# Optimization experiments

Measured on AMD Instinct MI355X. Metric: run time of the kernel, lower is better.

The kernel has to match this reference:

```python
import jax, jax.numpy as jnp
import numpy as np

N = 100000
E = 3200000
N_IN = 256
N_OUT = 256


def setup_inputs() -> dict:
    key = jax.random.key(0)
    k1, k2, k3, k4, k5, k6 = jax.random.split(key, 6)
    x = jax.random.normal(k1, (N, N_IN), dtype=jnp.float32)
    edge_row = jax.random.randint(k2, (E,), 0, N, dtype=jnp.int32)
    edge_col = jax.random.randint(k3, (E,), 0, N, dtype=jnp.int32)
    edge_val = jax.random.uniform(k4, (E,), dtype=jnp.float32)
    # nn.Linear(n_in, n_out): weight [n_out, n_in], bias [n_out]
    bound = 1.0 / np.sqrt(N_IN)
    W = jax.random.uniform(k5, (N_OUT, N_IN), minval=-bound, maxval=bound, dtype=jnp.float32)
    b = jax.random.uniform(k6, (N_OUT,), minval=-bound, maxval=bound, dtype=jnp.float32)
    return {"x": x, "edge_row": edge_row, "edge_col": edge_col, "edge_val": edge_val, "W": W, "b": b}


def reference(x, edge_row, edge_col, edge_val, W, b):
    # linear projection: [N, n_out]
    h = x @ W.T + b
    # sparse adj @ h via gather + segment-sum: out[r] = sum_e val_e * h[c_e]
    msg = edge_val[:, None] * h[edge_col]          # [E, n_out]
    agg = jax.ops.segment_sum(msg, edge_row, num_segments=N)  # [N, n_out]
    return jax.nn.elu(agg)
```

## Files before the change

### kernel.cpp

```cpp
#include <hip/hip_runtime.h>
#include <hip/hip_bf16.h>


#define NF 256
#define NBLK 256
#define BSHIFT 9
#define BROWS 512
#define NBUCK_MAX 256
#define YSTR 264

typedef unsigned short u16;
typedef unsigned int u32;
typedef __attribute__((ext_vector_type(8))) short bf16x8;
typedef __attribute__((ext_vector_type(8))) u16 u16x8;
typedef __attribute__((ext_vector_type(4))) float f32x4;

__device__ __forceinline__ u16 f2bf(float f) {
    unsigned u = __float_as_uint(f);
    u = (u + 0x7fffu + ((u >> 16) & 1u)) >> 16;
    return (u16)u;
}
__device__ __forceinline__ float bf2f(u16 h) {
    return __uint_as_float(((unsigned)h) << 16);
}

__global__ __launch_bounds__(256) void cvt_kernel(const float* __restrict__ in,
                                                  u16* __restrict__ outv, long n) {
    long i = ((long)blockIdx.x * blockDim.x + threadIdx.x) * 4;
    long stride = (long)gridDim.x * blockDim.x * 4;
    for (; i < n; i += stride) {
        float4 f = *(const float4*)(in + i);
        ushort4 o;
        o.x = f2bf(f.x); o.y = f2bf(f.y); o.z = f2bf(f.z); o.w = f2bf(f.w);
        *(ushort4*)(outv + i) = o;
    }
}

__global__ __launch_bounds__(256) void quant_kernel(const float* __restrict__ x,
                                                    char* __restrict__ xq,
                                                    float* __restrict__ sarr, int n) {
    int wv = (int)(((long)blockIdx.x * 256 + threadIdx.x) >> 6);
    int lane = threadIdx.x & 63;
    if (wv >= n) return;
    const float* xp = x + (size_t)wv * NF;
    float4 f = *(const float4*)(xp + lane * 4);
    float m = fmaxf(fmaxf(fabsf(f.x), fabsf(f.y)), fmaxf(fabsf(f.z), fabsf(f.w)));
    #pragma unroll
    for (int off = 32; off; off >>= 1) m = fmaxf(m, __shfl_xor(m, off));
    float mm = fmaxf(m, 1e-20f);
    float rs = 127.f / mm;
    char4 q;
    q.x = (char)__float2int_rn(f.x * rs);
    q.y = (char)__float2int_rn(f.y * rs);
    q.z = (char)__float2int_rn(f.z * rs);
    q.w = (char)__float2int_rn(f.w * rs);
    ((char4*)(xq + (size_t)wv * NF))[lane] = q;
    if (lane == 0) sarr[wv] = mm / 127.f;
}

__global__ __launch_bounds__(256) void hist_kernel(const int* __restrict__ erow,
                                                   int* __restrict__ histG,
                                                   int E, int chunk, int nbuck) {
    __shared__ int h[NBUCK_MAX];
    int b = blockIdx.x, tid = threadIdx.x;
    for (int i = tid; i < nbuck; i += 256) h[i] = 0;
    __syncthreads();
    int s = b * chunk, e = min(E, s + chunk);
    for (int i = s + tid; i < e; i += 256)
        atomicAdd(&h[erow[i] >> BSHIFT], 1);
    __syncthreads();
    for (int i = tid; i < nbuck; i += 256) histG[i * NBLK + b] = h[i];
}

__global__ __launch_bounds__(256) void scanA(int* __restrict__ data,
                                             int* __restrict__ bsum, int n) {
    __shared__ int s[256];
    int tid = threadIdx.x;
    int i = blockIdx.x * 256 + tid;
    int v = (i < n) ? data[i] : 0;
    s[tid] = v;
    __syncthreads();
    #pragma unroll
    for (int off = 1; off < 256; off <<= 1) {
        int t = (tid >= off) ? s[tid - off] : 0;
        __syncthreads();
        s[tid] += t;
        __syncthreads();
    }
    if (i < n) data[i] = s[tid] - v;
    if (tid == 255) bsum[blockIdx.x] = s[255];
}

__global__ __launch_bounds__(512) void scanB(const int* __restrict__ bsum,
                                             int* __restrict__ boff, int nb,
                                             int* __restrict__ total_out) {
    __shared__ int s[512];
    int tid = threadIdx.x;
    int v = (tid < nb) ? bsum[tid] : 0;
    s[tid] = v;
    __syncthreads();
    #pragma unroll
    for (int off = 1; off < 512; off <<= 1) {
        int t = (tid >= off) ? s[tid - off] : 0;
        __syncthreads();
        s[tid] += t;
        __syncthreads();
    }
    if (tid < nb) boff[tid] = s[tid] - v;
    if (tid == 511) *total_out = s[511];
}

__global__ __launch_bounds__(256) void scanC(int* __restrict__ data,
                                             const int* __restrict__ boff, int n) {
    int i = blockIdx.x * 256 + threadIdx.x;
    if (i < n) data[i] += boff[blockIdx.x];
}

__global__ __launch_bounds__(256) void binscatter_kernel(
        const int* __restrict__ erow, const int* __restrict__ ecol,
        const float* __restrict__ eval, const int* __restrict__ histGs,
        int2* __restrict__ tmp, int E, int chunk, int nbuck) {
    __shared__ int cur[NBUCK_MAX];
    int b = blockIdx.x, tid = threadIdx.x;
    for (int i = tid; i < nbuck; i += 256) cur[i] = histGs[i * NBLK + b];
    __syncthreads();
    int s = b * chunk, e = min(E, s + chunk);
    for (int i = s + tid; i < e; i += 256) {
        int r = erow[i];
        int k = r >> BSHIFT;
        int pos = atomicAdd(&cur[k], 1);
        tmp[pos] = make_int2((r & (BROWS - 1)) | (ecol[i] << BSHIFT),
                             __float_as_int(eval[i]));
    }
}

__global__ __launch_bounds__(256) void cluster_fill_kernel(
        const int2* __restrict__ tmp, const int* __restrict__ histGs,
        int* __restrict__ row_ptr, u32* __restrict__ rec,
        int N, int E, int nbuck) {
    __shared__ int cnt[BROWS];
    __shared__ int cur[BROWS];
    int k = blockIdx.x, tid = threadIdx.x;
    int base = k << BSHIFT;
    int nrows = min(BROWS, N - base);
    int tstart = histGs[k * NBLK];
    int tend = (k + 1 < nbuck) ? histGs[(k + 1) * NBLK] : E;

    for (int i = tid; i < BROWS; i += 256) cnt[i] = 0;
    __syncthreads();
    for (int j = tstart + tid; j < tend; j += 256)
        atomicAdd(&cnt[((u32)tmp[j].x) & (BROWS - 1)], 1);
    __syncthreads();
    cur[tid] = cnt[tid];
    cur[tid + 256] = cnt[tid + 256];
    __syncthreads();
    #pragma unroll
    for (int off = 1; off < BROWS; off <<= 1) {
        int i0 = tid, i1 = tid + 256;
        int t0 = (i0 >= off) ? cur[i0 - off] : 0;
        int t1 = (i1 >= off) ? cur[i1 - off] : 0;
        __syncthreads();
        cur[i0] += t0; cur[i1] += t1;
        __syncthreads();
    }
    #pragma unroll
    for (int p = 0; p < 2; ++p) {
        int i = tid + p * 256;
        int excl = tstart + cur[i] - cnt[i];
        if (i < nrows) row_ptr[base + i] = excl;
        cur[i] = excl;
    }
    if (k == nbuck - 1 && tid == 0) row_ptr[N] = E;
    __syncthreads();
    for (int j = tstart + tid; j < tend; j += 256) {
        int2 t = tmp[j];
        u32 w = (u32)t.x;
        int rl = w & (BROWS - 1);
        u32 c = w >> BSHIFT;
        float v = __int_as_float(t.y);
        int v15 = (int)(v * 32768.f + 0.5f);
        if (v15 > 32767) v15 = 32767;
        int pos = atomicAdd(&cur[rl], 1);
        rec[pos] = c | ((u32)v15 << 17);
    }
}

#define ACCQ(hh, vv)                                                         \
    a0 += (vv) * (float)(char)((hh).x);        a1 += (vv) * (float)(char)((hh).x >> 8); \
    a2 += (vv) * (float)(char)((hh).x >> 16);  a3 += (vv) * (float)(char)((hh).x >> 24); \
    a4 += (vv) * (float)(char)((hh).y);        a5 += (vv) * (float)(char)((hh).y >> 8); \
    a6 += (vv) * (float)(char)((hh).y >> 16);  a7 += (vv) * (float)(char)((hh).y >> 24);

__global__ __launch_bounds__(512) void fused_kernel(
        const char* __restrict__ xq, const float* __restrict__ sarr,
        const int* __restrict__ row_ptr, const u32* __restrict__ rec,
        const u16* __restrict__ Wb, const float* __restrict__ bias,
        float* __restrict__ out, int n) {
    __shared__ u16 ys[16 * YSTR];
    __shared__ float ss[16];
    int tid = threadIdx.x;
    int wid = tid >> 6;
    int lane = tid & 63;
    int half = lane >> 5;
    int fl = lane & 31;
    int rbase = blockIdx.x * 16;
    const float VS = 1.f / 32768.f;
    const char* xbase = xq + fl * 8;

    #pragma unroll
    for (int rr = 0; rr < 2; ++rr) {
        int lr = wid * 2 + rr;
        int row = rbase + lr;
        int start = 0, end = 0;
        if (row < n) { start = row_ptr[row]; end = row_ptr[row + 1]; }
        float a0 = 0.f, a1 = 0.f, a2 = 0.f, a3 = 0.f;
        float a4 = 0.f, a5 = 0.f, a6 = 0.f, a7 = 0.f;
        float sv = 0.f;
        int j = start;
        for (; j + 8 <= end; j += 8) {
            u32 w0 = rec[j + half];
            u32 w1 = rec[j + 2 + half];
            u32 w2 = rec[j + 4 + half];
            u32 w3 = rec[j + 6 + half];
            u32 c0 = w0 & 0x1FFFF, c1 = w1 & 0x1FFFF;
            u32 c2 = w2 & 0x1FFFF, c3 = w3 & 0x1FFFF;
            uint2 h0 = *(const uint2*)(xbase + (size_t)c0 * NF);
            uint2 h1 = *(const uint2*)(xbase + (size_t)c1 * NF);
            uint2 h2 = *(const uint2*)(xbase + (size_t)c2 * NF);
            uint2 h3 = *(const uint2*)(xbase + (size_t)c3 * NF);
            float s0 = sarr[c0], s1 = sarr[c1], s2 = sarr[c2], s3 = sarr[c3];
            float v0 = (float)(w0 >> 17) * VS;
            float v1 = (float)(w1 >> 17) * VS;
            float v2 = (float)(w2 >> 17) * VS;
            float v3 = (float)(w3 >> 17) * VS;
            sv += (v0 + v1) + (v2 + v3);
            float g0 = v0 * s0, g1 = v1 * s1, g2 = v2 * s2, g3 = v3 * s3;
            ACCQ(h0, g0); ACCQ(h1, g1); ACCQ(h2, g2); ACCQ(h3, g3);
        }
        for (int jj = j + half; jj < end; jj += 2) {
            u32 w = rec[jj];
            u32 c = w & 0x1FFFF;
            uint2 h = *(const uint2*)(xbase + (size_t)c * NF);
            float v = (float)(w >> 17) * VS;
            float g = v * sarr[c];
            sv += v;
            ACCQ(h, g);
        }
        a0 += __shfl_xor(a0, 32); a1 += __shfl_xor(a1, 32);
        a2 += __shfl_xor(a2, 32); a3 += __shfl_xor(a3, 32);
        a4 += __shfl_xor(a4, 32); a5 += __shfl_xor(a5, 32);
        a6 += __shfl_xor(a6, 32); a7 += __shfl_xor(a7, 32);
        sv += __shfl_xor(sv, 32);
        if (half == 0) {
            u16x8 p;
            p[0] = f2bf(a0); p[1] = f2bf(a1); p[2] = f2bf(a2); p[3] = f2bf(a3);
            p[4] = f2bf(a4); p[5] = f2bf(a5); p[6] = f2bf(a6); p[7] = f2bf(a7);
            *(u16x8*)(&ys[lr * YSTR + fl * 8]) = p;
            if (fl == 0) ss[lr] = sv;
        }
    }
    __syncthreads();

    int lrow = lane & 15;
    int kgrp = lane >> 4;
    bf16x8 af[8];
    #pragma unroll
    for (int ks = 0; ks < 8; ++ks)
        af[ks] = *(const bf16x8*)(&ys[lrow * YSTR + ks * 32 + kgrp * 8]);
    float sj[4];
    #pragma unroll
    for (int r = 0; r < 4; ++r) sj[r] = ss[kgrp * 4 + r];

    #pragma unroll
    for (int t = 0; t < 2; ++t) {
        int o0 = wid * 32 + t * 16;
        const u16* wrow = Wb + (size_t)(o0 + lrow) * NF + kgrp * 8;
        f32x4 acc = {0.f, 0.f, 0.f, 0.f};
        #pragma unroll
        for (int ks = 0; ks < 8; ++ks) {
            bf16x8 bf = *(const bf16x8*)(wrow + ks * 32);
            acc = __builtin_amdgcn_mfma_f32_16x16x32_bf16(af[ks], bf, acc, 0, 0, 0);
        }
        float bo = bias[o0 + lrow];
        #pragma unroll
        for (int r = 0; r < 4; ++r) {
            int grow = rbase + kgrp * 4 + r;
            if (grow < n) {
                float v = acc[r] + sj[r] * bo;
                out[(size_t)grow * NF + o0 + lrow] = (v > 0.f) ? v : (__expf(v) - 1.f);
            }
        }
    }
}

__global__ __launch_bounds__(256) void agg_f32_kernel(
        const float* __restrict__ xf, const int* __restrict__ row_ptr,
        const u32* __restrict__ rec, float* __restrict__ yf,
        float* __restrict__ svec, int n) {
    int wv = (int)(((long)blockIdx.x * 256 + threadIdx.x) >> 6);
    int lane = threadIdx.x & 63;
    if (wv >= n) return;
    int start = row_ptr[wv];
    int end = row_ptr[wv + 1];
    const float VS = 1.f / 32768.f;
    const float4* xv = (const float4*)xf;
    float4 acc = make_float4(0.f, 0.f, 0.f, 0.f);
    float sv = 0.f;
    for (int j = start; j < end; ++j) {
        u32 w = rec[j];
        float v = (float)(w >> 17) * VS;
        float4 h = xv[(size_t)(w & 0x1FFFF) * 64 + lane];
        acc.x += v * h.x; acc.y += v * h.y;
        acc.z += v * h.z; acc.w += v * h.w;
        sv += v;
    }
    *(float4*)(yf + (size_t)wv * NF + lane * 4) = acc;
    if (lane == 0) svec[wv] = sv;
}

__global__ __launch_bounds__(256) void gemm_elu_f32_kernel(
        float* __restrict__ out, const u16* __restrict__ Wb,
        const float* __restrict__ bias, const float* __restrict__ svec, int n) {
    int wid = threadIdx.x >> 6;
    int lane = threadIdx.x & 63;
    int lrow = lane & 15;
    int kgrp = lane >> 4;
    int r0 = blockIdx.x * 128 + wid * 32;
    if (r0 >= n) return;
    int rowA = min(r0 + lrow, n - 1);
    int rowB = min(r0 + 16 + lrow, n - 1);
    bf16x8 afA[8], afB[8];
    const float* yA = (const float*)out + (size_t)rowA * NF;
    const float* yB = (const float*)out + (size_t)rowB * NF;
    #pragma unroll
    for (int ks = 0; ks < 8; ++ks) {
        int k0 = ks * 32 + kgrp * 8;
        float4 f0 = *(const float4*)(yA + k0);
        float4 f1 = *(const float4*)(yA + k0 + 4);
        bf16x8 a;
        a[0] = (short)f2bf(f0.x); a[1] = (short)f2bf(f0.y);
        a[2] = (short)f2bf(f0.z); a[3] = (short)f2bf(f0.w);
        a[4] = (short)f2bf(f1.x); a[5] = (short)f2bf(f1.y);
        a[6] = (short)f2bf(f1.z); a[7] = (short)f2bf(f1.w);
        afA[ks] = a;
        f0 = *(const float4*)(yB + k0);
        f1 = *(const float4*)(yB + k0 + 4);
        a[0] = (short)f2bf(f0.x); a[1] = (short)f2bf(f0.y);
        a[2] = (short)f2bf(f0.z); a[3] = (short)f2bf(f0.w);
        a[4] = (short)f2bf(f1.x); a[5] = (short)f2bf(f1.y);
        a[6] = (short)f2bf(f1.z); a[7] = (short)f2bf(f1.w);
        afB[ks] = a;
    }
    float sjA[4], sjB[4];
    #pragma unroll
    for (int r = 0; r < 4; ++r) {
        sjA[r] = svec[min(r0 + kgrp * 4 + r, n - 1)];
        sjB[r] = svec[min(r0 + 16 + kgrp * 4 + r, n - 1)];
    }
    for (int ot = 0; ot < 16; ++ot) {
        int o0 = ot * 16;
        const u16* wrow = Wb + (size_t)(o0 + lrow) * NF + kgrp * 8;
        f32x4 accA = {0.f, 0.f, 0.f, 0.f};
        f32x4 accB = {0.f, 0.f, 0.f, 0.f};
        #pragma unroll
        for (int ks = 0; ks < 8; ++ks) {
            bf16x8 bf = *(const bf16x8*)(wrow + ks * 32);
            accA = __builtin_amdgcn_mfma_f32_16x16x32_bf16(afA[ks], bf, accA, 0, 0, 0);
            accB = __builtin_amdgcn_mfma_f32_16x16x32_bf16(afB[ks], bf, accB, 0, 0, 0);
        }
        float bo = bias[o0 + lrow];
        #pragma unroll
        for (int r = 0; r < 4; ++r) {
            int ra = r0 + kgrp * 4 + r;
            if (ra < n) {
                float v = accA[r] + sjA[r] * bo;
                out[(size_t)ra * NF + o0 + lrow] = (v > 0.f) ? v : (__expf(v) - 1.f);
            }
            int rb = r0 + 16 + kgrp * 4 + r;
            if (rb < n) {
                float v = accB[r] + sjB[r] * bo;
                out[(size_t)rb * NF + o0 + lrow] = (v > 0.f) ? v : (__expf(v) - 1.f);
            }
        }
    }
}

extern "C" void kernel_launch(void* const* d_in, const int* in_sizes, int n_in,
                              void* d_out, int out_size, void* d_ws, size_t ws_size,
                              hipStream_t stream) {
    const float* x        = (const float*)d_in[0];
    const int*   edge_row = (const int*)d_in[1];
    const int*   edge_col = (const int*)d_in[2];
    const float* edge_val = (const float*)d_in[3];
    const float* W        = (const float*)d_in[4];
    const float* b        = (const float*)d_in[5];
    float* out = (float*)d_out;

    const int N = in_sizes[0] / NF;
    const int E = in_sizes[1];
    const int nbuck = (N + BROWS - 1) >> BSHIFT;
    const int chunk = (E + NBLK - 1) / NBLK;

    size_t off = 0;
    char* base = (char*)d_ws;
    auto take = [&](size_t bytes) -> char* {
        char* q = base + off;
        off += (bytes + 255) & ~(size_t)255;
        return q;
    };
    u32*   rec     = (u32*)take((size_t)E * 4);
    int*   row_ptr = (int*)take((size_t)(N + 1) * 4);
    int*   histG   = (int*)take((size_t)nbuck * NBLK * 4);
    int*   bsum    = (int*)take(1024 * 4);
    int*   boff    = (int*)take(1024 * 4);
    int*   scr     = (int*)take(256);
    float* svec    = (float*)take((size_t)N * 4);
    u16*   Wb      = (u16*)take((size_t)NF * NF * 2);
    float* sarr    = (float*)take((size_t)N * 4);
    int2*  tmp     = (int2*)take((size_t)E * 8);
    size_t preQ = off;
    char*  xq      = (char*)take((size_t)N * NF);
    bool useQ = off <= ws_size;
    (void)preQ;

    const int nHist = nbuck * NBLK;
    const int nHistBlk = (nHist + 255) / 256;

    cvt_kernel<<<64, 256, 0, stream>>>(W, Wb, (long)NF * NF);

    if (useQ)
        quant_kernel<<<(N + 3) / 4, 256, 0, stream>>>(x, xq, sarr, N);

    hist_kernel<<<NBLK, 256, 0, stream>>>(edge_row, histG, E, chunk, nbuck);
    scanA<<<nHistBlk, 256, 0, stream>>>(histG, bsum, nHist);
    scanB<<<1, 512, 0, stream>>>(bsum, boff, nHistBlk, scr);
    scanC<<<nHistBlk, 256, 0, stream>>>(histG, boff, nHist);
    binscatter_kernel<<<NBLK, 256, 0, stream>>>(edge_row, edge_col, edge_val,
                                                histG, tmp, E, chunk, nbuck);
    cluster_fill_kernel<<<nbuck, 256, 0, stream>>>(tmp, histG, row_ptr, rec,
                                                   N, E, nbuck);

    if (useQ) {
        fused_kernel<<<(N + 15) / 16, 512, 0, stream>>>(xq, sarr, row_ptr, rec,
                                                        Wb, b, out, N);
    } else {
        agg_f32_kernel<<<(N + 3) / 4, 256, 0, stream>>>(x, row_ptr, rec, out,
                                                        svec, N);
        gemm_elu_f32_kernel<<<(N + 127) / 128, 256, 0, stream>>>(out, Wb, b,
                                                                 svec, N);
    }
}
```

Measured before the change: 372.2 us.

## Sort edges by column segment within row buckets and fuse prep kernels

The edge binning key becomes (row bucket, column segment), so within each row bucket the edges are grouped by column range. This is meant to improve gather locality of quantized feature rows during aggregation. The quantize, weight-convert and histogram kernels are merged into one launch to cut launch overhead. The prefix scan gains an extra level to handle the larger histogram. Features switch to unsigned 8-bit with a +128 offset that is subtracted after accumulation, which makes the byte-to-float conversion cheaper. In exchange, the histogram is much larger (4096 keys in shared memory per block) and the scan chain now has more launches.

```diff
diff --git a/kernel.cpp b/kernel.cpp
--- a/kernel.cpp
+++ b/kernel.cpp
@@ -6,11 +6,13 @@
 #define NBLK 256
 #define BSHIFT 9
 #define BROWS 512
-#define NBUCK_MAX 256
+#define SEGSHIFT 13
+#define NKEY_MAX 4096
 #define YSTR 264
 
 typedef unsigned short u16;
 typedef unsigned int u32;
+typedef unsigned char u8;
 typedef __attribute__((ext_vector_type(8))) short bf16x8;
 typedef __attribute__((ext_vector_type(8))) u16 u16x8;
 typedef __attribute__((ext_vector_type(4))) float f32x4;
@@ -20,8 +22,55 @@
     u = (u + 0x7fffu + ((u >> 16) & 1u)) >> 16;
     return (u16)u;
 }
-__device__ __forceinline__ float bf2f(u16 h) {
-    return __uint_as_float(((unsigned)h) << 16);
+
+__global__ __launch_bounds__(256) void prep_kernel(
+        const float* __restrict__ x, u8* __restrict__ xq,
+        float* __restrict__ sarr, int n,
+        const float* __restrict__ W, u16* __restrict__ Wb,
+        const int* __restrict__ erow, const int* __restrict__ ecol,
+        int* __restrict__ histG, int E, int chunk, int nkeys, int nseg) {
+    __shared__ int h[NKEY_MAX];
+    int b = blockIdx.x, tid = threadIdx.x;
+    int QB = (n + 3) / 4;
+    if (b < QB) {
+        int wv = b * 4 + (tid >> 6);
+        int lane = tid & 63;
+        if (wv >= n) return;
+        const float* xp = x + (size_t)wv * NF;
+        float4 f = *(const float4*)(xp + lane * 4);
+        float m = fmaxf(fmaxf(fabsf(f.x), fabsf(f.y)),
+                        fmaxf(fabsf(f.z), fabsf(f.w)));
+        #pragma unroll
+        for (int off = 32; off; off >>= 1) m = fmaxf(m, __shfl_xor(m, off));
+        float mm = fmaxf(m, 1e-20f);
+        float rs = 127.f / mm;
+        uchar4 q;
+        q.x = (u8)(__float2int_rn(f.x * rs) + 128);
+        q.y = (u8)(__float2int_rn(f.y * rs) + 128);
+        q.z = (u8)(__float2int_rn(f.z * rs) + 128);
+        q.w = (u8)(__float2int_rn(f.w * rs) + 128);
+        ((uchar4*)(xq + (size_t)wv * NF))[lane] = q;
+        if (lane == 0) sarr[wv] = mm / 127.f;
+    } else if (b < QB + 64) {
+        long i = ((long)(b - QB) * 256 + tid) * 4;
+        if (i < (long)NF * NF) {
+            float4 f = *(const float4*)(W + i);
+            ushort4 o;
+            o.x = f2bf(f.x); o.y = f2bf(f.y); o.z = f2bf(f.z); o.w = f2bf(f.w);
+            *(ushort4*)(Wb + i) = o;
+        }
+    } else {
+        int hb = b - QB - 64;
+        for (int i = tid; i < nkeys; i += 256) h[i] = 0;
+        __syncthreads();
+        int s = hb * chunk, e = min(E, s + chunk);
+        for (int i = s + tid; i < e; i += 256) {
+            int key = (erow[i] >> BSHIFT) * nseg + (ecol[i] >> SEGSHIFT);
+            atomicAdd(&h[key], 1);
+        }
+        __syncthreads();
+        for (int i = tid; i < nkeys; i += 256) histG[i * NBLK + hb] = h[i];
+    }
 }
 
 __global__ __launch_bounds__(256) void cvt_kernel(const float* __restrict__ in,
@@ -36,40 +85,20 @@
     }
 }
 
-__global__ __launch_bounds__(256) void quant_kernel(const float* __restrict__ x,
-                                                    char* __restrict__ xq,
-                                                    float* __restrict__ sarr, int n) {
-    int wv = (int)(((long)blockIdx.x * 256 + threadIdx.x) >> 6);
-    int lane = threadIdx.x & 63;
-    if (wv >= n) return;
-    const float* xp = x + (size_t)wv * NF;
-    float4 f = *(const float4*)(xp + lane * 4);
-    float m = fmaxf(fmaxf(fabsf(f.x), fabsf(f.y)), fmaxf(fabsf(f.z), fabsf(f.w)));
-    #pragma unroll
-    for (int off = 32; off; off >>= 1) m = fmaxf(m, __shfl_xor(m, off));
-    float mm = fmaxf(m, 1e-20f);
-    float rs = 127.f / mm;
-    char4 q;
-    q.x = (char)__float2int_rn(f.x * rs);
-    q.y = (char)__float2int_rn(f.y * rs);
-    q.z = (char)__float2int_rn(f.z * rs);
-    q.w = (char)__float2int_rn(f.w * rs);
-    ((char4*)(xq + (size_t)wv * NF))[lane] = q;
-    if (lane == 0) sarr[wv] = mm / 127.f;
-}
-
-__global__ __launch_bounds__(256) void hist_kernel(const int* __restrict__ erow,
-                                                   int* __restrict__ histG,
-                                                   int E, int chunk, int nbuck) {
-    __shared__ int h[NBUCK_MAX];
+__global__ __launch_bounds__(256) void hist_kernel(
+        const int* __restrict__ erow, const int* __restrict__ ecol,
+        int* __restrict__ histG, int E, int chunk, int nkeys, int nseg) {
+    __shared__ int h[NKEY_MAX];
     int b = blockIdx.x, tid = threadIdx.x;
-    for (int i = tid; i < nbuck; i += 256) h[i] = 0;
+    for (int i = tid; i < nkeys; i += 256) h[i] = 0;
     __syncthreads();
     int s = b * chunk, e = min(E, s + chunk);
-    for (int i = s + tid; i < e; i += 256)
-        atomicAdd(&h[erow[i] >> BSHIFT], 1);
-    __syncthreads();
-    for (int i = tid; i < nbuck; i += 256) histG[i * NBLK + b] = h[i];
+    for (int i = s + tid; i < e; i += 256) {
+        int key = (erow[i] >> BSHIFT) * nseg + (ecol[i] >> SEGSHIFT);
+        atomicAdd(&h[key], 1);
+    }
+    __syncthreads();
+    for (int i = tid; i < nkeys; i += 256) histG[i * NBLK + b] = h[i];
 }
 
 __global__ __launch_bounds__(256) void scanA(int* __restrict__ data,
@@ -119,17 +148,18 @@
 __global__ __launch_bounds__(256) void binscatter_kernel(
         const int* __restrict__ erow, const int* __restrict__ ecol,
         const float* __restrict__ eval, const int* __restrict__ histGs,
-        int2* __restrict__ tmp, int E, int chunk, int nbuck) {
-    __shared__ int cur[NBUCK_MAX];
+        int2* __restrict__ tmp, int E, int chunk, int nkeys, int nseg) {
+    __shared__ int cur[NKEY_MAX];
     int b = blockIdx.x, tid = threadIdx.x;
-    for (int i = tid; i < nbuck; i += 256) cur[i] = histGs[i * NBLK + b];
+    for (int i = tid; i < nkeys; i += 256) cur[i] = histGs[i * NBLK + b];
     __syncthreads();
     int s = b * chunk, e = min(E, s + chunk);
     for (int i = s + tid; i < e; i += 256) {
         int r = erow[i];
-        int k = r >> BSHIFT;
-        int pos = atomicAdd(&cur[k], 1);
-        tmp[pos] = make_int2((r & (BROWS - 1)) | (ecol[i] << BSHIFT),
+        int c = ecol[i];
+        int key = (r >> BSHIFT) * nseg + (c >> SEGSHIFT);
+        int pos = atomicAdd(&cur[key], 1);
+        tmp[pos] = make_int2((r & (BROWS - 1)) | (c << BSHIFT),
                              __float_as_int(eval[i]));
     }
 }
@@ -137,14 +167,14 @@
 __global__ __launch_bounds__(256) void cluster_fill_kernel(
         const int2* __restrict__ tmp, const int* __restrict__ histGs,
         int* __restrict__ row_ptr, u32* __restrict__ rec,
-        int N, int E, int nbuck) {
+        int N, int E, int nbuck, int nseg) {
     __shared__ int cnt[BROWS];
     __shared__ int cur[BROWS];
     int k = blockIdx.x, tid = threadIdx.x;
     int base = k << BSHIFT;
     int nrows = min(BROWS, N - base);
-    int tstart = histGs[k * NBLK];
-    int tend = (k + 1 < nbuck) ? histGs[(k + 1) * NBLK] : E;
+    int tstart = histGs[(k * nseg) * NBLK];
+    int tend = (k + 1 < nbuck) ? histGs[((k + 1) * nseg) * NBLK] : E;
 
     for (int i = tid; i < BROWS; i += 256) cnt[i] = 0;
     __syncthreads();
@@ -185,14 +215,19 @@
     }
 }
 
-#define ACCQ(hh, vv)                                                         \
-    a0 += (vv) * (float)(char)((hh).x);        a1 += (vv) * (float)(char)((hh).x >> 8); \
-    a2 += (vv) * (float)(char)((hh).x >> 16);  a3 += (vv) * (float)(char)((hh).x >> 24); \
-    a4 += (vv) * (float)(char)((hh).y);        a5 += (vv) * (float)(char)((hh).y >> 8); \
-    a6 += (vv) * (float)(char)((hh).y >> 16);  a7 += (vv) * (float)(char)((hh).y >> 24);
+#define ACCU(hh, gg)                                                          \
+    a0 += (gg) * (float)((hh).x & 0xffu);                                     \
+    a1 += (gg) * (float)(((hh).x >> 8) & 0xffu);                              \
+    a2 += (gg) * (float)(((hh).x >> 16) & 0xffu);                             \
+    a3 += (gg) * (float)((hh).x >> 24);                                       \
+    a4 += (gg) * (float)((hh).y & 0xffu);                                     \
+    a5 += (gg) * (float)(((hh).y >> 8) & 0xffu);                              \
+    a6 += (gg) * (float)(((hh).y >> 16) & 0xffu);                             \
+    a7 += (gg) * (float)((hh).y >> 24);                                       \
+    t  += (gg);
 
 __global__ __launch_bounds__(512) void fused_kernel(
-        const char* __restrict__ xq, const float* __restrict__ sarr,
+        const u8* __restrict__ xq, const float* __restrict__ sarr,
         const int* __restrict__ row_ptr, const u32* __restrict__ rec,
         const u16* __restrict__ Wb, const float* __restrict__ bias,
         float* __restrict__ out, int n) {
@@ -205,7 +240,7 @@
     int fl = lane & 31;
     int rbase = blockIdx.x * 16;
     const float VS = 1.f / 32768.f;
-    const char* xbase = xq + fl * 8;
+    const u8* xbase = xq + fl * 8;
 
     #pragma unroll
     for (int rr = 0; rr < 2; ++rr) {
@@ -215,7 +250,7 @@
         if (row < n) { start = row_ptr[row]; end = row_ptr[row + 1]; }
         float a0 = 0.f, a1 = 0.f, a2 = 0.f, a3 = 0.f;
         float a4 = 0.f, a5 = 0.f, a6 = 0.f, a7 = 0.f;
-        float sv = 0.f;
+        float sv = 0.f, t = 0.f;
         int j = start;
         for (; j + 8 <= end; j += 8) {
             u32 w0 = rec[j + half];
@@ -235,7 +270,7 @@
             float v3 = (float)(w3 >> 17) * VS;
             sv += (v0 + v1) + (v2 + v3);
             float g0 = v0 * s0, g1 = v1 * s1, g2 = v2 * s2, g3 = v3 * s3;
-            ACCQ(h0, g0); ACCQ(h1, g1); ACCQ(h2, g2); ACCQ(h3, g3);
+            ACCU(h0, g0); ACCU(h1, g1); ACCU(h2, g2); ACCU(h3, g3);
         }
         for (int jj = j + half; jj < end; jj += 2) {
             u32 w = rec[jj];
@@ -244,8 +279,11 @@
             float v = (float)(w >> 17) * VS;
             float g = v * sarr[c];
             sv += v;
-            ACCQ(h, g);
-        }
+            ACCU(h, g);
+        }
+        float t128 = 128.f * t;
+        a0 -= t128; a1 -= t128; a2 -= t128; a3 -= t128;
+        a4 -= t128; a5 -= t128; a6 -= t128; a7 -= t128;
         a0 += __shfl_xor(a0, 32); a1 += __shfl_xor(a1, 32);
         a2 += __shfl_xor(a2, 32); a3 += __shfl_xor(a3, 32);
         a4 += __shfl_xor(a4, 32); a5 += __shfl_xor(a5, 32);
@@ -399,6 +437,8 @@
     const int N = in_sizes[0] / NF;
     const int E = in_sizes[1];
     const int nbuck = (N + BROWS - 1) >> BSHIFT;
+    const int nseg  = (N + (1 << SEGSHIFT) - 1) >> SEGSHIFT;
+    const int nkeys = nbuck * nseg;
     const int chunk = (E + NBLK - 1) / NBLK;
 
     size_t off = 0;
@@ -410,35 +450,43 @@
     };
     u32*   rec     = (u32*)take((size_t)E * 4);
     int*   row_ptr = (int*)take((size_t)(N + 1) * 4);
-    int*   histG   = (int*)take((size_t)nbuck * NBLK * 4);
-    int*   bsum    = (int*)take(1024 * 4);
-    int*   boff    = (int*)take(1024 * 4);
+    int*   histG   = (int*)take((size_t)nkeys * NBLK * 4);
+    int*   bsum1   = (int*)take((size_t)((nkeys * NBLK + 255) / 256) * 4);
+    int*   bsum2   = (int*)take(1024 * 4);
+    int*   boff2   = (int*)take(1024 * 4);
     int*   scr     = (int*)take(256);
     float* svec    = (float*)take((size_t)N * 4);
     u16*   Wb      = (u16*)take((size_t)NF * NF * 2);
     float* sarr    = (float*)take((size_t)N * 4);
     int2*  tmp     = (int2*)take((size_t)E * 8);
-    size_t preQ = off;
-    char*  xq      = (char*)take((size_t)N * NF);
+    u8*    xq      = (u8*)take((size_t)N * NF);
     bool useQ = off <= ws_size;
-    (void)preQ;
-
-    const int nHist = nbuck * NBLK;
-    const int nHistBlk = (nHist + 255) / 256;
-
-    cvt_kernel<<<64, 256, 0, stream>>>(W, Wb, (long)NF * NF);
-
-    if (useQ)
-        quant_kernel<<<(N + 3) / 4, 256, 0, stream>>>(x, xq, sarr, N);
-
-    hist_kernel<<<NBLK, 256, 0, stream>>>(edge_row, histG, E, chunk, nbuck);
-    scanA<<<nHistBlk, 256, 0, stream>>>(histG, bsum, nHist);
-    scanB<<<1, 512, 0, stream>>>(bsum, boff, nHistBlk, scr);
-    scanC<<<nHistBlk, 256, 0, stream>>>(histG, boff, nHist);
+
+    const int nHist = nkeys * NBLK;
+    const int nb1 = (nHist + 255) / 256;
+    const int nb2 = (nb1 + 255) / 256;
+
+    if (useQ) {
+        int QB = (N + 3) / 4;
+        prep_kernel<<<QB + 64 + NBLK, 256, 0, stream>>>(
+            x, xq, sarr, N, W, Wb, edge_row, edge_col, histG, E, chunk,
+            nkeys, nseg);
+    } else {
+        cvt_kernel<<<64, 256, 0, stream>>>(W, Wb, (long)NF * NF);
+        hist_kernel<<<NBLK, 256, 0, stream>>>(edge_row, edge_col, histG, E,
+                                              chunk, nkeys, nseg);
+    }
+
+    scanA<<<nb1, 256, 0, stream>>>(histG, bsum1, nHist);
+    scanA<<<nb2, 256, 0, stream>>>(bsum1, bsum2, nb1);
+    scanB<<<1, 512, 0, stream>>>(bsum2, boff2, nb2, scr);
+    scanC<<<nb2, 256, 0, stream>>>(bsum1, boff2, nb1);
+    scanC<<<nb1, 256, 0, stream>>>(histG, bsum1, nHist);
+
     binscatter_kernel<<<NBLK, 256, 0, stream>>>(edge_row, edge_col, edge_val,
-                                                histG, tmp, E, chunk, nbuck);
+                                                histG, tmp, E, chunk, nkeys, nseg);
     cluster_fill_kernel<<<nbuck, 256, 0, stream>>>(tmp, histG, row_ptr, rec,
-                                                   N, E, nbuck);
+                                                   N, E, nbuck, nseg);
 
     if (useQ) {
         fused_kernel<<<(N + 15) / 16, 512, 0, stream>>>(xq, sarr, row_ptr, rec,
```

New measurement: 406.7 us. 1.09x slower.

## Fuse prep kernels and shrink edge bucket temp to packed u32 plus u16

Applied to the files above, without the earlier changes.

Quantization of x, the W to bf16 conversion and the edge-row histogram now run as one launch, with blocks partitioned by role, instead of three separate kernels. The binning scatter now writes the final packed record (column plus 15-bit value) and a separate u16 local row, replacing the 8-byte int2 temp. The fill kernel therefore reads 6 bytes per edge instead of 8 and copies the record directly. The fill kernel also uses 512 threads so each thread owns one row slot. This cuts launch overhead and intermediate traffic, at the cost of two scattered writes per edge in binscatter.

```diff
diff --git a/kernel.cpp b/kernel.cpp
--- a/kernel.cpp
+++ b/kernel.cpp
@@ -11,6 +11,7 @@
 
 typedef unsigned short u16;
 typedef unsigned int u32;
+typedef unsigned char u8;
 typedef __attribute__((ext_vector_type(8))) short bf16x8;
 typedef __attribute__((ext_vector_type(8))) u16 u16x8;
 typedef __attribute__((ext_vector_type(4))) float f32x4;
@@ -20,8 +21,53 @@
     u = (u + 0x7fffu + ((u >> 16) & 1u)) >> 16;
     return (u16)u;
 }
-__device__ __forceinline__ float bf2f(u16 h) {
-    return __uint_as_float(((unsigned)h) << 16);
+
+__global__ __launch_bounds__(256) void prep_kernel(
+        const float* __restrict__ x, char* __restrict__ xq,
+        float* __restrict__ sarr, int n,
+        const float* __restrict__ W, u16* __restrict__ Wb,
+        const int* __restrict__ erow, int* __restrict__ histG,
+        int E, int chunk, int nbuck) {
+    __shared__ int h[NBUCK_MAX];
+    int b = blockIdx.x, tid = threadIdx.x;
+    int QB = (n + 3) / 4;
+    if (b < QB) {
+        int wv = b * 4 + (tid >> 6);
+        int lane = tid & 63;
+        if (wv >= n) return;
+        const float* xp = x + (size_t)wv * NF;
+        float4 f = *(const float4*)(xp + lane * 4);
+        float m = fmaxf(fmaxf(fabsf(f.x), fabsf(f.y)),
+                        fmaxf(fabsf(f.z), fabsf(f.w)));
+        #pragma unroll
+        for (int off = 32; off; off >>= 1) m = fmaxf(m, __shfl_xor(m, off));
+        float mm = fmaxf(m, 1e-20f);
+        float rs = 127.f / mm;
+        char4 q;
+        q.x = (char)__float2int_rn(f.x * rs);
+        q.y = (char)__float2int_rn(f.y * rs);
+        q.z = (char)__float2int_rn(f.z * rs);
+        q.w = (char)__float2int_rn(f.w * rs);
+        ((char4*)(xq + (size_t)wv * NF))[lane] = q;
+        if (lane == 0) sarr[wv] = mm / 127.f;
+    } else if (b < QB + 64) {
+        long i = ((long)(b - QB) * 256 + tid) * 4;
+        if (i < (long)NF * NF) {
+            float4 f = *(const float4*)(W + i);
+            ushort4 o;
+            o.x = f2bf(f.x); o.y = f2bf(f.y); o.z = f2bf(f.z); o.w = f2bf(f.w);
+            *(ushort4*)(Wb + i) = o;
+        }
+    } else {
+        int hb = b - QB - 64;
+        for (int i = tid; i < nbuck; i += 256) h[i] = 0;
+        __syncthreads();
+        int s = hb * chunk, e = min(E, s + chunk);
+        for (int i = s + tid; i < e; i += 256)
+            atomicAdd(&h[erow[i] >> BSHIFT], 1);
+        __syncthreads();
+        for (int i = tid; i < nbuck; i += 256) histG[i * NBLK + hb] = h[i];
+    }
 }
 
 __global__ __launch_bounds__(256) void cvt_kernel(const float* __restrict__ in,
@@ -36,28 +82,6 @@
     }
 }
 
-__global__ __launch_bounds__(256) void quant_kernel(const float* __restrict__ x,
-                                                    char* __restrict__ xq,
-                                                    float* __restrict__ sarr, int n) {
-    int wv = (int)(((long)blockIdx.x * 256 + threadIdx.x) >> 6);
-    int lane = threadIdx.x & 63;
-    if (wv >= n) return;
-    const float* xp = x + (size_t)wv * NF;
-    float4 f = *(const float4*)(xp + lane * 4);
-    float m = fmaxf(fmaxf(fabsf(f.x), fabsf(f.y)), fmaxf(fabsf(f.z), fabsf(f.w)));
-    #pragma unroll
-    for (int off = 32; off; off >>= 1) m = fmaxf(m, __shfl_xor(m, off));
-    float mm = fmaxf(m, 1e-20f);
-    float rs = 127.f / mm;
-    char4 q;
-    q.x = (char)__float2int_rn(f.x * rs);
-    q.y = (char)__float2int_rn(f.y * rs);
-    q.z = (char)__float2int_rn(f.z * rs);
-    q.w = (char)__float2int_rn(f.w * rs);
-    ((char4*)(xq + (size_t)wv * NF))[lane] = q;
-    if (lane == 0) sarr[wv] = mm / 127.f;
-}
-
 __global__ __launch_bounds__(256) void hist_kernel(const int* __restrict__ erow,
                                                    int* __restrict__ histG,
                                                    int E, int chunk, int nbuck) {
@@ -119,7 +143,8 @@
 __global__ __launch_bounds__(256) void binscatter_kernel(
         const int* __restrict__ erow, const int* __restrict__ ecol,
         const float* __restrict__ eval, const int* __restrict__ histGs,
-        int2* __restrict__ tmp, int E, int chunk, int nbuck) {
+        u32* __restrict__ tmp4, u16* __restrict__ rowlo,
+        int E, int chunk, int nbuck) {
     __shared__ int cur[NBUCK_MAX];
     int b = blockIdx.x, tid = threadIdx.x;
     for (int i = tid; i < nbuck; i += 256) cur[i] = histGs[i * NBLK + b];
@@ -128,16 +153,19 @@
     for (int i = s + tid; i < e; i += 256) {
         int r = erow[i];
         int k = r >> BSHIFT;
+        float v = eval[i];
+        int v15 = (int)(v * 32768.f + 0.5f);
+        if (v15 > 32767) v15 = 32767;
         int pos = atomicAdd(&cur[k], 1);
-        tmp[pos] = make_int2((r & (BROWS - 1)) | (ecol[i] << BSHIFT),
-                             __float_as_int(eval[i]));
-    }
-}
-
-__global__ __launch_bounds__(256) void cluster_fill_kernel(
-        const int2* __restrict__ tmp, const int* __restrict__ histGs,
-        int* __restrict__ row_ptr, u32* __restrict__ rec,
-        int N, int E, int nbuck) {
+        tmp4[pos] = (u32)ecol[i] | ((u32)v15 << 17);
+        rowlo[pos] = (u16)(r & (BROWS - 1));
+    }
+}
+
+__global__ __launch_bounds__(512) void cluster_fill_kernel(
+        const u32* __restrict__ tmp4, const u16* __restrict__ rowlo,
+        const int* __restrict__ histGs, int* __restrict__ row_ptr,
+        u32* __restrict__ rec, int N, int E, int nbuck) {
     __shared__ int cnt[BROWS];
     __shared__ int cur[BROWS];
     int k = blockIdx.x, tid = threadIdx.x;
@@ -146,42 +174,29 @@
     int tstart = histGs[k * NBLK];
     int tend = (k + 1 < nbuck) ? histGs[(k + 1) * NBLK] : E;
 
-    for (int i = tid; i < BROWS; i += 256) cnt[i] = 0;
-    __syncthreads();
-    for (int j = tstart + tid; j < tend; j += 256)
-        atomicAdd(&cnt[((u32)tmp[j].x) & (BROWS - 1)], 1);
+    cnt[tid] = 0;
+    __syncthreads();
+    for (int j = tstart + tid; j < tend; j += 512)
+        atomicAdd(&cnt[rowlo[j]], 1);
     __syncthreads();
     cur[tid] = cnt[tid];
-    cur[tid + 256] = cnt[tid + 256];
     __syncthreads();
     #pragma unroll
     for (int off = 1; off < BROWS; off <<= 1) {
-        int i0 = tid, i1 = tid + 256;
-        int t0 = (i0 >= off) ? cur[i0 - off] : 0;
-        int t1 = (i1 >= off) ? cur[i1 - off] : 0;
-        __syncthreads();
-        cur[i0] += t0; cur[i1] += t1;
-        __syncthreads();
-    }
-    #pragma unroll
-    for (int p = 0; p < 2; ++p) {
-        int i = tid + p * 256;
-        int excl = tstart + cur[i] - cnt[i];
-        if (i < nrows) row_ptr[base + i] = excl;
-        cur[i] = excl;
-    }
+        int t = (tid >= off) ? cur[tid - off] : 0;
+        __syncthreads();
+        cur[tid] += t;
+        __syncthreads();
+    }
+    int excl = tstart + cur[tid] - cnt[tid];
+    if (tid < nrows) row_ptr[base + tid] = excl;
+    cur[tid] = excl;
     if (k == nbuck - 1 && tid == 0) row_ptr[N] = E;
     __syncthreads();
-    for (int j = tstart + tid; j < tend; j += 256) {
-        int2 t = tmp[j];
-        u32 w = (u32)t.x;
-        int rl = w & (BROWS - 1);
-        u32 c = w >> BSHIFT;
-        float v = __int_as_float(t.y);
-        int v15 = (int)(v * 32768.f + 0.5f);
-        if (v15 > 32767) v15 = 32767;
+    for (int j = tstart + tid; j < tend; j += 512) {
+        int rl = rowlo[j];
         int pos = atomicAdd(&cur[rl], 1);
-        rec[pos] = c | ((u32)v15 << 17);
+        rec[pos] = tmp4[j];
     }
 }
 
@@ -417,28 +432,31 @@
     float* svec    = (float*)take((size_t)N * 4);
     u16*   Wb      = (u16*)take((size_t)NF * NF * 2);
     float* sarr    = (float*)take((size_t)N * 4);
-    int2*  tmp     = (int2*)take((size_t)E * 8);
-    size_t preQ = off;
+    u32*   tmp4    = (u32*)take((size_t)E * 4);
+    u16*   rowlo   = (u16*)take((size_t)E * 2);
     char*  xq      = (char*)take((size_t)N * NF);
     bool useQ = off <= ws_size;
-    (void)preQ;
 
     const int nHist = nbuck * NBLK;
-    const int nHistBlk = (nHist + 255) / 256;
-
-    cvt_kernel<<<64, 256, 0, stream>>>(W, Wb, (long)NF * NF);
-
-    if (useQ)
-        quant_kernel<<<(N + 3) / 4, 256, 0, stream>>>(x, xq, sarr, N);
-
-    hist_kernel<<<NBLK, 256, 0, stream>>>(edge_row, histG, E, chunk, nbuck);
-    scanA<<<nHistBlk, 256, 0, stream>>>(histG, bsum, nHist);
-    scanB<<<1, 512, 0, stream>>>(bsum, boff, nHistBlk, scr);
-    scanC<<<nHistBlk, 256, 0, stream>>>(histG, boff, nHist);
+    const int nb1 = (nHist + 255) / 256;
+
+    if (useQ) {
+        int QB = (N + 3) / 4;
+        prep_kernel<<<QB + 64 + NBLK, 256, 0, stream>>>(
+            x, xq, sarr, N, W, Wb, edge_row, histG, E, chunk, nbuck);
+    } else {
+        cvt_kernel<<<64, 256, 0, stream>>>(W, Wb, (long)NF * NF);
+        hist_kernel<<<NBLK, 256, 0, stream>>>(edge_row, histG, E, chunk, nbuck);
+    }
+
+    scanA<<<nb1, 256, 0, stream>>>(histG, bsum, nHist);
+    scanB<<<1, 512, 0, stream>>>(bsum, boff, nb1, scr);
+    scanC<<<nb1, 256, 0, stream>>>(histG, boff, nHist);
+
     binscatter_kernel<<<NBLK, 256, 0, stream>>>(edge_row, edge_col, edge_val,
-                                                histG, tmp, E, chunk, nbuck);
-    cluster_fill_kernel<<<nbuck, 256, 0, stream>>>(tmp, histG, row_ptr, rec,
-                                                   N, E, nbuck);
+                                                histG, tmp4, rowlo, E, chunk, nbuck);
+    cluster_fill_kernel<<<nbuck, 512, 0, stream>>>(tmp4, rowlo, histG, row_ptr,
+                                                   rec, N, E, nbuck);
 
     if (useQ) {
         fused_kernel<<<(N + 15) / 16, 512, 0, stream>>>(xq, sarr, row_ptr, rec,
```

Result: no change. 369.2 us (-0.8%).
